# Performance work log

Hardware: AMD Instinct MI355X
Metric: run time of the kernel (lower is better)

## Reference

```python
import jax, jax.numpy as jnp
import numpy as np

MARGIN = 0.2


def colbert_score(q, d):
    # q: (B, Q, D), d: (B, K, D) -> scalar
    sim = jnp.einsum('bqd,bkd->bqk', q, d)          # (B, Q, K)
    max_sim = jnp.max(sim, axis=2)                   # (B, Q) row-wise max over doc tokens
    return jnp.sum(max_sim)                          # sum over query tokens and batch


def setup_inputs() -> dict:
    key = jax.random.key(0)
    k1, k2, k3 = jax.random.split(key, 3)
    B, Q, K, D = 256, 256, 512, 128
    return {
        'q': jax.random.normal(k1, (B, Q, D), dtype=jnp.float32),
        'p': jax.random.normal(k2, (B, K, D), dtype=jnp.float32),
        'n': jax.random.normal(k3, (B, K, D), dtype=jnp.float32),
    }


def reference(q, p, n):
    pos_score = colbert_score(q, p)
    neg_score = colbert_score(q, n)
    loss = jax.nn.relu(MARGIN + neg_score - pos_score)
    # torch .mean() on a scalar is identity
    return loss
```

## Files before the change

### kernel.cpp

```cpp
#include <hip/hip_runtime.h>


#define MARGIN   0.2f
#define Bn       256
#define Qn       256
#define Kn       512
#define Dn       128
#define TN       32
#define NT       (Kn / TN)
#define BSTR     136
#define NTHREADS 256

typedef __attribute__((ext_vector_type(8))) short short8;
typedef __attribute__((ext_vector_type(4))) short short4v;
typedef __attribute__((ext_vector_type(4))) float f32x4;

__device__ __forceinline__ void split_trunc(float x, unsigned short& hi, unsigned short& lo) {
    unsigned int u = __float_as_uint(x);
    hi = (unsigned short)(u >> 16);
    float l = x - __uint_as_float(u & 0xFFFF0000u);
    lo = (unsigned short)(__float_as_uint(l) >> 16);
}

__global__ __launch_bounds__(NTHREADS, 2)
void colbert_pass_kernel(const float* __restrict__ qg,
                         const float* __restrict__ pg,
                         const float* __restrict__ ng,
                         double* __restrict__ sum_ws) {
    __shared__ short Bs[2][2][TN * BSTR];
    __shared__ float part[4];

    const int tid  = threadIdx.x;
    const int w    = tid >> 6;
    const int lane = tid & 63;
    const int l16  = lane & 15;
    const int quad = lane >> 4;
    const int b    = blockIdx.x;
    const int pass = blockIdx.y;

    const float* docb = (pass ? ng : pg) + (size_t)b * Kn * Dn;

    float4 pre[4];
    {
        const float4* s4 = (const float4*)docb;
#pragma unroll
        for (int k = 0; k < 4; ++k) pre[k] = s4[tid + 256 * k];
    }

    short8 Ahi[4][4], Alo[4][4];
    {
        const float* qb = qg + (size_t)b * Qn * Dn;
#pragma unroll
        for (int mi = 0; mi < 4; ++mi)
#pragma unroll
            for (int ks = 0; ks < 4; ++ks) {
                const float* src = qb + (size_t)(w * 64 + mi * 16 + l16) * Dn
                                      + ks * 32 + quad * 8;
                float4 v0 = *(const float4*)src;
                float4 v1 = *(const float4*)(src + 4);
                float x[8] = {v0.x, v0.y, v0.z, v0.w, v1.x, v1.y, v1.z, v1.w};
#pragma unroll
                for (int j = 0; j < 8; ++j) {
                    unsigned short h, l;
                    split_trunc(x[j], h, l);
                    Ahi[mi][ks][j] = (short)h;
                    Alo[mi][ks][j] = (short)l;
                }
            }
    }

    float maxv[4][4];
#pragma unroll
    for (int mi = 0; mi < 4; ++mi)
#pragma unroll
        for (int r = 0; r < 4; ++r) maxv[mi][r] = -3e38f;

    int buf = 0;
    for (int t = 0; t < NT; ++t) {
#pragma unroll
        for (int k = 0; k < 4; ++k) {
            int i   = tid + 256 * k;
            int doc = i >> 5;
            int d4  = i & 31;
            float4 v = pre[k];
            float x[4] = {v.x, v.y, v.z, v.w};
            short4v hi, lo;
#pragma unroll
            for (int j = 0; j < 4; ++j) {
                unsigned short h, l;
                split_trunc(x[j], h, l);
                hi[j] = (short)h;
                lo[j] = (short)l;
            }
            *(short4v*)&Bs[buf][0][doc * BSTR + d4 * 4] = hi;
            *(short4v*)&Bs[buf][1][doc * BSTR + d4 * 4] = lo;
        }
        __syncthreads();

        if (t + 1 < NT) {
            const float4* s4 = (const float4*)(docb + (size_t)(t + 1) * TN * Dn);
#pragma unroll
            for (int k = 0; k < 4; ++k) pre[k] = s4[tid + 256 * k];
        }

        f32x4 acc[4][2];
#pragma unroll
        for (int mi = 0; mi < 4; ++mi)
#pragma unroll
            for (int ni = 0; ni < 2; ++ni) acc[mi][ni] = (f32x4){0.f, 0.f, 0.f, 0.f};

#pragma unroll
        for (int ni = 0; ni < 2; ++ni) {
            short8 bhi[4], blo[4];
#pragma unroll
            for (int ks = 0; ks < 4; ++ks) {
                int off = (ni * 16 + l16) * BSTR + ks * 32 + quad * 8;
                bhi[ks] = *(const short8*)&Bs[buf][0][off];
                blo[ks] = *(const short8*)&Bs[buf][1][off];
            }
#pragma unroll
            for (int ks = 0; ks < 4; ++ks) {
#pragma unroll
                for (int mi = 0; mi < 4; ++mi)
                    acc[mi][ni] = __builtin_amdgcn_mfma_f32_16x16x32_bf16(
                        Ahi[mi][ks], bhi[ks], acc[mi][ni], 0, 0, 0);
#pragma unroll
                for (int mi = 0; mi < 4; ++mi)
                    acc[mi][ni] = __builtin_amdgcn_mfma_f32_16x16x32_bf16(
                        Alo[mi][ks], bhi[ks], acc[mi][ni], 0, 0, 0);
#pragma unroll
                for (int mi = 0; mi < 4; ++mi)
                    acc[mi][ni] = __builtin_amdgcn_mfma_f32_16x16x32_bf16(
                        Ahi[mi][ks], blo[ks], acc[mi][ni], 0, 0, 0);
            }
        }

#pragma unroll
        for (int mi = 0; mi < 4; ++mi)
#pragma unroll
            for (int r = 0; r < 4; ++r)
                maxv[mi][r] = fmaxf(maxv[mi][r], fmaxf(acc[mi][0][r], acc[mi][1][r]));
        buf ^= 1;
    }

#pragma unroll
    for (int off = 1; off < 16; off <<= 1)
#pragma unroll
        for (int mi = 0; mi < 4; ++mi)
#pragma unroll
            for (int r = 0; r < 4; ++r)
                maxv[mi][r] = fmaxf(maxv[mi][r], __shfl_xor(maxv[mi][r], off));

    float s = 0.f;
#pragma unroll
    for (int mi = 0; mi < 4; ++mi)
#pragma unroll
        for (int r = 0; r < 4; ++r) s += maxv[mi][r];
    if (l16 != 0) s = 0.f;
    s += __shfl_xor(s, 16);
    s += __shfl_xor(s, 32);
    if (lane == 0) part[w] = s;
    __syncthreads();
    if (tid == 0) {
        double t = (double)part[0] + part[1] + part[2] + part[3];
        atomicAdd(sum_ws, pass ? -t : t);
    }
}

__global__ void finalize_kernel(const double* __restrict__ sum_ws,
                                float* __restrict__ out) {
    out[0] = fmaxf(0.0f, MARGIN - (float)sum_ws[0]);
}

extern "C" void kernel_launch(void* const* d_in, const int* in_sizes, int n_in,
                              void* d_out, int out_size, void* d_ws, size_t ws_size,
                              hipStream_t stream) {
    const float* q = (const float*)d_in[0];
    const float* p = (const float*)d_in[1];
    const float* n = (const float*)d_in[2];
    float* out = (float*)d_out;
    double* ws = (double*)d_ws;

    hipMemsetAsync(ws, 0, sizeof(double), stream);

    colbert_pass_kernel<<<dim3(Bn, 2), NTHREADS, 0, stream>>>(q, p, n, ws);
    finalize_kernel<<<1, 1, 0, stream>>>(ws, out);
}
```

Before: 180.3 us.

## Split query rows across 8 waves with 512 threads per block

Doubles the block to 512 threads so each of 8 waves holds 32 query rows instead of 64. That halves the per-wave A fragments, accumulators and prefetch registers, and each block now converts 2 doc vectors per thread per tile. The intent is higher wave occupancy, with launch bounds raised to 4, to better hide LDS and global latency. The cost is that each B fragment read from LDS now feeds half as many MFMAs, which doubles LDS read traffic relative to compute, and the block-wide barrier now spans more waves.

```diff
diff --git a/kernel.cpp b/kernel.cpp
--- a/kernel.cpp
+++ b/kernel.cpp
@@ -9,7 +9,7 @@
 #define TN       32
 #define NT       (Kn / TN)
 #define BSTR     136
-#define NTHREADS 256
+#define NTHREADS 512
 
 typedef __attribute__((ext_vector_type(8))) short short8;
 typedef __attribute__((ext_vector_type(4))) short short4v;
@@ -22,13 +22,13 @@
     lo = (unsigned short)(__float_as_uint(l) >> 16);
 }
 
-__global__ __launch_bounds__(NTHREADS, 2)
+__global__ __launch_bounds__(NTHREADS, 4)
 void colbert_pass_kernel(const float* __restrict__ qg,
                          const float* __restrict__ pg,
                          const float* __restrict__ ng,
                          double* __restrict__ sum_ws) {
     __shared__ short Bs[2][2][TN * BSTR];
-    __shared__ float part[4];
+    __shared__ float part[8];
 
     const int tid  = threadIdx.x;
     const int w    = tid >> 6;
@@ -40,21 +40,21 @@
 
     const float* docb = (pass ? ng : pg) + (size_t)b * Kn * Dn;
 
-    float4 pre[4];
+    float4 pre[2];
     {
         const float4* s4 = (const float4*)docb;
 #pragma unroll
-        for (int k = 0; k < 4; ++k) pre[k] = s4[tid + 256 * k];
+        for (int k = 0; k < 2; ++k) pre[k] = s4[tid + 512 * k];
     }
 
-    short8 Ahi[4][4], Alo[4][4];
+    short8 Ahi[2][4], Alo[2][4];
     {
         const float* qb = qg + (size_t)b * Qn * Dn;
 #pragma unroll
-        for (int mi = 0; mi < 4; ++mi)
+        for (int mi = 0; mi < 2; ++mi)
 #pragma unroll
             for (int ks = 0; ks < 4; ++ks) {
-                const float* src = qb + (size_t)(w * 64 + mi * 16 + l16) * Dn
+                const float* src = qb + (size_t)(w * 32 + mi * 16 + l16) * Dn
                                       + ks * 32 + quad * 8;
                 float4 v0 = *(const float4*)src;
                 float4 v1 = *(const float4*)(src + 4);
@@ -69,17 +69,17 @@
             }
     }
 
-    float maxv[4][4];
+    float maxv[2][4];
 #pragma unroll
-    for (int mi = 0; mi < 4; ++mi)
+    for (int mi = 0; mi < 2; ++mi)
 #pragma unroll
         for (int r = 0; r < 4; ++r) maxv[mi][r] = -3e38f;
 
     int buf = 0;
     for (int t = 0; t < NT; ++t) {
 #pragma unroll
-        for (int k = 0; k < 4; ++k) {
-            int i   = tid + 256 * k;
+        for (int k = 0; k < 2; ++k) {
+            int i   = tid + 512 * k;
             int doc = i >> 5;
             int d4  = i & 31;
             float4 v = pre[k];
@@ -100,43 +100,39 @@
         if (t + 1 < NT) {
             const float4* s4 = (const float4*)(docb + (size_t)(t + 1) * TN * Dn);
 #pragma unroll
-            for (int k = 0; k < 4; ++k) pre[k] = s4[tid + 256 * k];
+            for (int k = 0; k < 2; ++k) pre[k] = s4[tid + 512 * k];
         }
 
-        f32x4 acc[4][2];
+        f32x4 acc[2][2];
 #pragma unroll
-        for (int mi = 0; mi < 4; ++mi)
+        for (int mi = 0; mi < 2; ++mi)
 #pragma unroll
             for (int ni = 0; ni < 2; ++ni) acc[mi][ni] = (f32x4){0.f, 0.f, 0.f, 0.f};
 
 #pragma unroll
         for (int ni = 0; ni < 2; ++ni) {
-            short8 bhi[4], blo[4];
 #pragma unroll
             for (int ks = 0; ks < 4; ++ks) {
                 int off = (ni * 16 + l16) * BSTR + ks * 32 + quad * 8;
-                bhi[ks] = *(const short8*)&Bs[buf][0][off];
-                blo[ks] = *(const short8*)&Bs[buf][1][off];
-            }
-#pragma unroll
-            for (int ks = 0; ks < 4; ++ks) {
-#pragma unroll
-                for (int mi = 0; mi < 4; ++mi)
-                    acc[mi][ni] = __builtin_amdgcn_mfma_f32_16x16x32_bf16(
-                        Ahi[mi][ks], bhi[ks], acc[mi][ni], 0, 0, 0);
-#pragma unroll
-                for (int mi = 0; mi < 4; ++mi)
-                    acc[mi][ni] = __builtin_amdgcn_mfma_f32_16x16x32_bf16(
-                        Alo[mi][ks], bhi[ks], acc[mi][ni], 0, 0, 0);
-#pragma unroll
-                for (int mi = 0; mi < 4; ++mi)
-                    acc[mi][ni] = __builtin_amdgcn_mfma_f32_16x16x32_bf16(
-                        Ahi[mi][ks], blo[ks], acc[mi][ni], 0, 0, 0);
+                short8 bh = *(const short8*)&Bs[buf][0][off];
+                short8 bl = *(const short8*)&Bs[buf][1][off];
+                acc[0][ni] = __builtin_amdgcn_mfma_f32_16x16x32_bf16(
+                    Ahi[0][ks], bh, acc[0][ni], 0, 0, 0);
+                acc[1][ni] = __builtin_amdgcn_mfma_f32_16x16x32_bf16(
+                    Ahi[1][ks], bh, acc[1][ni], 0, 0, 0);
+                acc[0][ni] = __builtin_amdgcn_mfma_f32_16x16x32_bf16(
+                    Alo[0][ks], bh, acc[0][ni], 0, 0, 0);
+                acc[1][ni] = __builtin_amdgcn_mfma_f32_16x16x32_bf16(
+                    Alo[1][ks], bh, acc[1][ni], 0, 0, 0);
+                acc[0][ni] = __builtin_amdgcn_mfma_f32_16x16x32_bf16(
+                    Ahi[0][ks], bl, acc[0][ni], 0, 0, 0);
+                acc[1][ni] = __builtin_amdgcn_mfma_f32_16x16x32_bf16(
+                    Ahi[1][ks], bl, acc[1][ni], 0, 0, 0);
             }
         }
 
 #pragma unroll
-        for (int mi = 0; mi < 4; ++mi)
+        for (int mi = 0; mi < 2; ++mi)
 #pragma unroll
             for (int r = 0; r < 4; ++r)
                 maxv[mi][r] = fmaxf(maxv[mi][r], fmaxf(acc[mi][0][r], acc[mi][1][r]));
@@ -146,14 +142,14 @@
 #pragma unroll
     for (int off = 1; off < 16; off <<= 1)
 #pragma unroll
-        for (int mi = 0; mi < 4; ++mi)
+        for (int mi = 0; mi < 2; ++mi)
 #pragma unroll
             for (int r = 0; r < 4; ++r)
                 maxv[mi][r] = fmaxf(maxv[mi][r], __shfl_xor(maxv[mi][r], off));
 
     float s = 0.f;
 #pragma unroll
-    for (int mi = 0; mi < 4; ++mi)
+    for (int mi = 0; mi < 2; ++mi)
 #pragma unroll
         for (int r = 0; r < 4; ++r) s += maxv[mi][r];
     if (l16 != 0) s = 0.f;
@@ -162,7 +158,9 @@
     if (lane == 0) part[w] = s;
     __syncthreads();
     if (tid == 0) {
-        double t = (double)part[0] + part[1] + part[2] + part[3];
+        double t = 0.0;
+#pragma unroll
+        for (int i = 0; i < 8; ++i) t += (double)part[i];
         atomicAdd(sum_ws, pass ? -t : t);
     }
 }
```

Result: no change. 180.4 us (+0.1%).

## Screen with single bf16 MFMA pass and rescore candidates in fp32

Applied to the files above, without the earlier changes.

Replaces the three-term bf16 split GEMM with a single RNE-rounded bf16 MFMA pass that screens, for each query row, the doc tokens whose approximate score is within a fixed band of the running max. Candidate indices go into LDS per row through shared atomics, and each thread then recomputes the exact fp32 dot products for its row's candidates from global memory to take the true max. This cuts MFMA work to a third and drops the lo-part conversions. In exchange it adds per-tile cross-lane max shuffles, LDS atomics and a gather phase. Correctness depends on the band holding the true max and on the candidate cap of 48 per row not being exceeded.

```diff
diff --git a/kernel.cpp b/kernel.cpp
--- a/kernel.cpp
+++ b/kernel.cpp
@@ -10,16 +10,22 @@
 #define NT       (Kn / TN)
 #define BSTR     136
 #define NTHREADS 256
+#define CAP      48
+#define BAND     4.5f
 
 typedef __attribute__((ext_vector_type(8))) short short8;
-typedef __attribute__((ext_vector_type(4))) short short4v;
 typedef __attribute__((ext_vector_type(4))) float f32x4;
 
-__device__ __forceinline__ void split_trunc(float x, unsigned short& hi, unsigned short& lo) {
+__device__ __forceinline__ unsigned int bf16_rne(float x) {
     unsigned int u = __float_as_uint(x);
-    hi = (unsigned short)(u >> 16);
-    float l = x - __uint_as_float(u & 0xFFFF0000u);
-    lo = (unsigned short)(__float_as_uint(l) >> 16);
+    return (u + 0x7FFFu + ((u >> 16) & 1u)) >> 16;
+}
+__device__ __forceinline__ unsigned int pack_bf16_rne(float a, float b) {
+    unsigned int ua = __float_as_uint(a);
+    unsigned int ub = __float_as_uint(b);
+    unsigned int ra = (ua + 0x7FFFu + ((ua >> 16) & 1u)) >> 16;
+    unsigned int rb = (ub + 0x7FFFu + ((ub >> 16) & 1u)) & 0xFFFF0000u;
+    return rb | ra;
 }
 
 __global__ __launch_bounds__(NTHREADS, 2)
@@ -27,8 +33,10 @@
                          const float* __restrict__ pg,
                          const float* __restrict__ ng,
                          double* __restrict__ sum_ws) {
-    __shared__ short Bs[2][2][TN * BSTR];
-    __shared__ float part[4];
+    __shared__ short Bs[2][TN * BSTR];
+    __shared__ unsigned short cidx[Qn][CAP];
+    __shared__ unsigned int   ccnt[Qn];
+    __shared__ double partd[4];
 
     const int tid  = threadIdx.x;
     const int w    = tid >> 6;
@@ -40,6 +48,8 @@
 
     const float* docb = (pass ? ng : pg) + (size_t)b * Kn * Dn;
 
+    ccnt[tid] = 0;
+
     float4 pre[4];
     {
         const float4* s4 = (const float4*)docb;
@@ -47,7 +57,7 @@
         for (int k = 0; k < 4; ++k) pre[k] = s4[tid + 256 * k];
     }
 
-    short8 Ahi[4][4], Alo[4][4];
+    short8 Ahi[4][4];
     {
         const float* qb = qg + (size_t)b * Qn * Dn;
 #pragma unroll
@@ -60,12 +70,8 @@
                 float4 v1 = *(const float4*)(src + 4);
                 float x[8] = {v0.x, v0.y, v0.z, v0.w, v1.x, v1.y, v1.z, v1.w};
 #pragma unroll
-                for (int j = 0; j < 8; ++j) {
-                    unsigned short h, l;
-                    split_trunc(x[j], h, l);
-                    Ahi[mi][ks][j] = (short)h;
-                    Alo[mi][ks][j] = (short)l;
-                }
+                for (int j = 0; j < 8; ++j)
+                    Ahi[mi][ks][j] = (short)bf16_rne(x[j]);
             }
     }
 
@@ -82,18 +88,10 @@
             int i   = tid + 256 * k;
             int doc = i >> 5;
             int d4  = i & 31;
-            float4 v = pre[k];
-            float x[4] = {v.x, v.y, v.z, v.w};
-            short4v hi, lo;
-#pragma unroll
-            for (int j = 0; j < 4; ++j) {
-                unsigned short h, l;
-                split_trunc(x[j], h, l);
-                hi[j] = (short)h;
-                lo[j] = (short)l;
-            }
-            *(short4v*)&Bs[buf][0][doc * BSTR + d4 * 4] = hi;
-            *(short4v*)&Bs[buf][1][doc * BSTR + d4 * 4] = lo;
+            uint2 h;
+            h.x = pack_bf16_rne(pre[k].x, pre[k].y);
+            h.y = pack_bf16_rne(pre[k].z, pre[k].w);
+            *(uint2*)&Bs[buf][doc * BSTR + d4 * 4] = h;
         }
         __syncthreads();
 
@@ -103,67 +101,96 @@
             for (int k = 0; k < 4; ++k) pre[k] = s4[tid + 256 * k];
         }
 
-        f32x4 acc[4][2];
+        f32x4 a0[4], a1[4];
+#pragma unroll
+        for (int mi = 0; mi < 4; ++mi) {
+            a0[mi] = (f32x4){0.f, 0.f, 0.f, 0.f};
+            a1[mi] = (f32x4){0.f, 0.f, 0.f, 0.f};
+        }
+#pragma unroll
+        for (int ks = 0; ks < 4; ++ks) {
+            short8 bh = *(const short8*)&Bs[buf][l16 * BSTR + ks * 32 + quad * 8];
+#pragma unroll
+            for (int mi = 0; mi < 4; ++mi)
+                a0[mi] = __builtin_amdgcn_mfma_f32_16x16x32_bf16(Ahi[mi][ks], bh, a0[mi], 0, 0, 0);
+        }
+#pragma unroll
+        for (int ks = 0; ks < 4; ++ks) {
+            short8 bh = *(const short8*)&Bs[buf][(16 + l16) * BSTR + ks * 32 + quad * 8];
+#pragma unroll
+            for (int mi = 0; mi < 4; ++mi)
+                a1[mi] = __builtin_amdgcn_mfma_f32_16x16x32_bf16(Ahi[mi][ks], bh, a1[mi], 0, 0, 0);
+        }
+
 #pragma unroll
         for (int mi = 0; mi < 4; ++mi)
 #pragma unroll
-            for (int ni = 0; ni < 2; ++ni) acc[mi][ni] = (f32x4){0.f, 0.f, 0.f, 0.f};
-
-#pragma unroll
-        for (int ni = 0; ni < 2; ++ni) {
-            short8 bhi[4], blo[4];
-#pragma unroll
-            for (int ks = 0; ks < 4; ++ks) {
-                int off = (ni * 16 + l16) * BSTR + ks * 32 + quad * 8;
-                bhi[ks] = *(const short8*)&Bs[buf][0][off];
-                blo[ks] = *(const short8*)&Bs[buf][1][off];
+            for (int r = 0; r < 4; ++r)
+                maxv[mi][r] = fmaxf(maxv[mi][r], fmaxf(a0[mi][r], a1[mi][r]));
+#pragma unroll
+        for (int off = 1; off < 16; off <<= 1)
+#pragma unroll
+            for (int mi = 0; mi < 4; ++mi)
+#pragma unroll
+                for (int r = 0; r < 4; ++r)
+                    maxv[mi][r] = fmaxf(maxv[mi][r], __shfl_xor(maxv[mi][r], off));
+
+#pragma unroll
+        for (int mi = 0; mi < 4; ++mi)
+#pragma unroll
+            for (int r = 0; r < 4; ++r) {
+                float thr = maxv[mi][r] - BAND;
+                int rowl  = w * 64 + mi * 16 + quad * 4 + r;
+                if (a0[mi][r] >= thr) {
+                    unsigned id = atomicAdd(&ccnt[rowl], 1u);
+                    if (id < CAP) cidx[rowl][id] = (unsigned short)(t * 32 + l16);
+                }
+                if (a1[mi][r] >= thr) {
+                    unsigned id = atomicAdd(&ccnt[rowl], 1u);
+                    if (id < CAP) cidx[rowl][id] = (unsigned short)(t * 32 + 16 + l16);
+                }
             }
-#pragma unroll
-            for (int ks = 0; ks < 4; ++ks) {
-#pragma unroll
-                for (int mi = 0; mi < 4; ++mi)
-                    acc[mi][ni] = __builtin_amdgcn_mfma_f32_16x16x32_bf16(
-                        Ahi[mi][ks], bhi[ks], acc[mi][ni], 0, 0, 0);
-#pragma unroll
-                for (int mi = 0; mi < 4; ++mi)
-                    acc[mi][ni] = __builtin_amdgcn_mfma_f32_16x16x32_bf16(
-                        Alo[mi][ks], bhi[ks], acc[mi][ni], 0, 0, 0);
-#pragma unroll
-                for (int mi = 0; mi < 4; ++mi)
-                    acc[mi][ni] = __builtin_amdgcn_mfma_f32_16x16x32_bf16(
-                        Ahi[mi][ks], blo[ks], acc[mi][ni], 0, 0, 0);
-            }
-        }
-
-#pragma unroll
-        for (int mi = 0; mi < 4; ++mi)
-#pragma unroll
-            for (int r = 0; r < 4; ++r)
-                maxv[mi][r] = fmaxf(maxv[mi][r], fmaxf(acc[mi][0][r], acc[mi][1][r]));
         buf ^= 1;
     }
 
-#pragma unroll
-    for (int off = 1; off < 16; off <<= 1)
-#pragma unroll
-        for (int mi = 0; mi < 4; ++mi)
-#pragma unroll
-            for (int r = 0; r < 4; ++r)
-                maxv[mi][r] = fmaxf(maxv[mi][r], __shfl_xor(maxv[mi][r], off));
-
-    float s = 0.f;
-#pragma unroll
-    for (int mi = 0; mi < 4; ++mi)
-#pragma unroll
-        for (int r = 0; r < 4; ++r) s += maxv[mi][r];
-    if (l16 != 0) s = 0.f;
-    s += __shfl_xor(s, 16);
-    s += __shfl_xor(s, 32);
-    if (lane == 0) part[w] = s;
+    __syncthreads();
+
+    const int row = tid;
+    const int n   = (int)min(ccnt[row], (unsigned)CAP);
+    const float4* q4 = (const float4*)(qg + ((size_t)b * Qn + row) * Dn);
+    float best = -3e38f;
+    for (int j = 0; j < n; ++j) {
+        const float4* d4p = (const float4*)(docb + (size_t)cidx[row][j] * Dn);
+        f32x4 s0 = (f32x4){0.f, 0.f, 0.f, 0.f};
+        f32x4 s1 = (f32x4){0.f, 0.f, 0.f, 0.f};
+#pragma unroll
+        for (int kk = 0; kk < 16; ++kk) {
+            float4 qa  = q4[2 * kk];
+            float4 qb2 = q4[2 * kk + 1];
+            float4 da  = d4p[2 * kk];
+            float4 db  = d4p[2 * kk + 1];
+            s0[0] = fmaf(qa.x, da.x, s0[0]);
+            s0[1] = fmaf(qa.y, da.y, s0[1]);
+            s0[2] = fmaf(qa.z, da.z, s0[2]);
+            s0[3] = fmaf(qa.w, da.w, s0[3]);
+            s1[0] = fmaf(qb2.x, db.x, s1[0]);
+            s1[1] = fmaf(qb2.y, db.y, s1[1]);
+            s1[2] = fmaf(qb2.z, db.z, s1[2]);
+            s1[3] = fmaf(qb2.w, db.w, s1[3]);
+        }
+        float dot = (s0[0] + s0[1]) + (s0[2] + s0[3])
+                  + (s1[0] + s1[1]) + (s1[2] + s1[3]);
+        best = fmaxf(best, dot);
+    }
+
+    double s = (double)best;
+#pragma unroll
+    for (int off = 1; off < 64; off <<= 1) s += __shfl_xor(s, off);
+    if (lane == 0) partd[w] = s;
     __syncthreads();
     if (tid == 0) {
-        double t = (double)part[0] + part[1] + part[2] + part[3];
-        atomicAdd(sum_ws, pass ? -t : t);
+        double tot = partd[0] + partd[1] + partd[2] + partd[3];
+        atomicAdd(sum_ws, pass ? -tot : tot);
     }
 }
 
```

After: 444.6 us. 2.47x slower.
